# Performance work log

Measured on AMD Instinct MI355X. Metric: run time of the kernel, lower is better.

The kernel has to match this reference:

```python
import jax, jax.numpy as jnp
import numpy as np

RADIUS = 0.1
NSAMPLE = 32


def setup_inputs() -> dict:
    key = jax.random.key(0)
    k1, k2, k3, k4 = jax.random.split(key, 4)
    B, N, C = 8, 8192, 64
    C_in = 3 + C  # relative xyz concatenated with features
    H1, H2 = 64, 128
    xyz = jax.random.uniform(k1, (B, N, 3), dtype=jnp.float32)  # points in unit cube
    features = jax.random.normal(k2, (B, C, N), dtype=jnp.float32)
    W1 = jax.random.normal(k3, (H1, C_in), dtype=jnp.float32) / np.sqrt(C_in)
    b1 = jnp.zeros((H1,), dtype=jnp.float32)
    W2 = jax.random.normal(k4, (H2, H1), dtype=jnp.float32) / np.sqrt(H1)
    b2 = jnp.zeros((H2,), dtype=jnp.float32)
    return {"xyz": xyz, "features": features, "W1": W1, "b1": b1,
            "W2": W2, "b2": b2, "npoint": 2048}


def _ball_query(xyz, new_xyz, radius, nsample):
    # xyz: (B,N,3), new_xyz: (B,S,3) -> idx (B,S,nsample) int32
    N = xyz.shape[1]
    d2 = jnp.sum((new_xyz[:, :, None, :] - xyz[:, None, :, :]) ** 2, axis=-1)  # (B,S,N)
    mask = d2 < radius * radius
    # sort key: in-ball points keep their index (ascending order first),
    # out-of-ball points pushed behind by +N
    ar = jnp.arange(N, dtype=jnp.int32)
    key = jnp.where(mask, ar, ar + N)
    idx_sorted = jnp.argsort(key, axis=-1)[..., :nsample].astype(jnp.int32)  # (B,S,ns)
    count = jnp.sum(mask, axis=-1)  # (B,S)
    first = idx_sorted[..., :1]
    slot = jnp.arange(nsample)
    # CUDA ball_query pads missing slots with the first found index
    return jnp.where(slot[None, None, :] < count[..., None], idx_sorted, first)


def reference(xyz, features, W1, b1, W2, b2, npoint):
    # use_fps=False: sample_idxs = arange(npoint) -> new_xyz = first npoint points
    new_xyz = xyz[:, :npoint, :]  # (B,S,3)
    idx = _ball_query(xyz, new_xyz, RADIUS, NSAMPLE)  # (B,S,ns)

    # QueryAndGroup: gather xyz (centered) + features, concat on channel dim
    gx = jax.vmap(lambda p, i: p[i])(xyz, idx)  # (B,S,ns,3)
    rel = gx - new_xyz[:, :, None, :]  # (B,S,ns,3)
    gf = jax.vmap(lambda f, i: f[:, i])(features, idx)  # (B,C,S,ns)
    grouped = jnp.concatenate([jnp.transpose(rel, (0, 3, 1, 2)), gf], axis=1)  # (B,3+C,S,ns)

    # SharedMLP: 1x1 conv + ReLU stack
    h = jax.nn.relu(jnp.einsum('oc,bcsn->bosn', W1, grouped) + b1[None, :, None, None])
    h = jax.nn.relu(jnp.einsum('oc,bcsn->bosn', W2, h) + b2[None, :, None, None])

    # max_pool2d over nsample, squeeze
    new_features = jnp.max(h, axis=-1)  # (B,H2,S)
    return new_xyz, new_features
```

## Files before the change

### kernel.cpp

```cpp
#include <hip/hip_runtime.h>
#include <hip/hip_bf16.h>

#define B_      8
#define N_      8192
#define C_      64
#define H1_     64
#define H2_     128
#define NS      32
#define NPOINT  2048
#define NGROUP  (B_ * NPOINT)
#define NXYZ    (B_ * NPOINT * 3)
#define GD      10
#define NCP     1024

typedef short bf16x8 __attribute__((ext_vector_type(8)));
typedef short bf16x4 __attribute__((ext_vector_type(4)));
typedef float f32x4  __attribute__((ext_vector_type(4)));

#define MFMA32 __builtin_amdgcn_mfma_f32_16x16x32_bf16
#define MFMA16 __builtin_amdgcn_mfma_f32_16x16x16bf16_1k

__device__ inline unsigned short f2bf(float f) {
    unsigned u = __builtin_bit_cast(unsigned, f);
    return (unsigned short)((u + 0x7FFF + ((u >> 16) & 1)) >> 16);
}
__device__ inline float bf2f(unsigned short h) {
    unsigned u = ((unsigned)h) << 16;
    return __builtin_bit_cast(float, u);
}

__global__ __launch_bounds__(256) void copy_newxyz_kernel(
    const float* __restrict__ xyz, float* __restrict__ out)
{
    int i = blockIdx.x * 256 + threadIdx.x;
    if (i < NXYZ) {
        int b = i / (NPOINT * 3);
        int r = i - b * (NPOINT * 3);
        out[i] = xyz[(size_t)b * N_ * 3 + r];
    }
}

__global__ __launch_bounds__(256) void prep_kernel(
    const float* __restrict__ W1, const float* __restrict__ W2,
    unsigned short* __restrict__ W1x_hi, unsigned short* __restrict__ W1x_lo,
    unsigned short* __restrict__ W2x_hi, unsigned short* __restrict__ W2x_lo)
{
    int t = blockIdx.x * 256 + threadIdx.x;
    if (t < 6144) {
        int j = t & 7, cl = (t >> 3) & 15, kq = (t >> 7) & 3, t2 = t >> 9;
        int kt = t2 % 3, mt = t2 / 3;
        int row = mt * 16 + cl, k = kt * 32 + kq * 8 + j;
        float wv = 0.f;
        if (k < 64) wv = W1[row * 67 + 3 + k];
        else if (k < 67) wv = W1[row * 67 + (k - 64)];
        unsigned short h = f2bf(wv);
        W1x_hi[t] = h; W1x_lo[t] = f2bf(wv - bf2f(h));
    }
    if (t < 8192) {
        int i = t & 3, half = (t >> 2) & 1, cl = (t >> 3) & 15;
        int kq = (t >> 7) & 3, kt2p = (t >> 9) & 1, mt = t >> 10;
        int row = mt * 16 + cl, k = kt2p * 32 + half * 16 + kq * 4 + i;
        float wv = W2[row * 64 + k];
        unsigned short h = f2bf(wv);
        W2x_hi[t] = h; W2x_lo[t] = f2bf(wv - bf2f(h));
    }
}

__global__ __launch_bounds__(256) void ftrans_kernel(
    const float* __restrict__ f,
    unsigned short* __restrict__ hi, unsigned short* __restrict__ lo)
{
    __shared__ float tile[64][65];
    int bidx = blockIdx.x;
    int b = bidx >> 7, nt = bidx & 127;
    int n0 = nt * 64;
    int tx = threadIdx.x & 63, ty = threadIdx.x >> 6;
#pragma unroll
    for (int k = 0; k < 16; ++k) {
        int c = ty * 16 + k;
        tile[c][tx] = f[((size_t)b * C_ + c) * N_ + n0 + tx];
    }
    __syncthreads();
#pragma unroll
    for (int k = 0; k < 16; ++k) {
        int n = ty * 16 + k;
        float v = tile[tx][n];
        unsigned short h = f2bf(v);
        size_t dst = ((size_t)(b * N_ + n0 + n)) * C_ + tx;
        hi[dst] = h;
        lo[dst] = f2bf(v - bf2f(h));
    }
}

__global__ __launch_bounds__(256) void gridbuild_kernel(
    const float* __restrict__ xyz,
    int* __restrict__ cellStart,
    int* __restrict__ sortedId,
    float* __restrict__ sortedXyz)
{
    __shared__ int hist[NCP];
    __shared__ int wsum[4];
    int b = blockIdx.x, t = threadIdx.x;
    for (int i = t; i < NCP; i += 256) hist[i] = 0;
    __syncthreads();
    const float* base = xyz + (size_t)b * N_ * 3;
    for (int k = 0; k < N_ / 256; ++k) {
        int i = k * 256 + t;
        float x = base[i * 3], y = base[i * 3 + 1], z = base[i * 3 + 2];
        int c = (((int)(x * 9.999f)) * GD + (int)(y * 9.999f)) * GD + (int)(z * 9.999f);
        atomicAdd(&hist[c], 1);
    }
    __syncthreads();
    int h0 = hist[t * 4], h1 = hist[t * 4 + 1], h2 = hist[t * 4 + 2], h3 = hist[t * 4 + 3];
    int s = h0 + h1 + h2 + h3;
    int lane = t & 63, w = t >> 6;
    int v = s;
    for (int d = 1; d < 64; d <<= 1) {
        int o = __shfl_up(v, d);
        if (lane >= d) v += o;
    }
    if (lane == 63) wsum[w] = v;
    __syncthreads();
    int wofs = 0;
    for (int i = 0; i < 4; ++i) wofs += (i < w) ? wsum[i] : 0;
    int excl = wofs + v - s;
    int* cs = cellStart + b * (NCP + 1);
    cs[t * 4]     = excl;
    cs[t * 4 + 1] = excl + h0;
    cs[t * 4 + 2] = excl + h0 + h1;
    cs[t * 4 + 3] = excl + h0 + h1 + h2;
    if (t == 255) cs[NCP] = excl + s;
    __syncthreads();
    hist[t * 4] = excl; hist[t * 4 + 1] = excl + h0;
    hist[t * 4 + 2] = excl + h0 + h1; hist[t * 4 + 3] = excl + h0 + h1 + h2;
    __syncthreads();
    for (int k = 0; k < N_ / 256; ++k) {
        int i = k * 256 + t;
        float x = base[i * 3], y = base[i * 3 + 1], z = base[i * 3 + 2];
        int c = (((int)(x * 9.999f)) * GD + (int)(y * 9.999f)) * GD + (int)(z * 9.999f);
        int pos = atomicAdd(&hist[c], 1);
        sortedId[b * N_ + pos] = i;
        float* d = sortedXyz + ((size_t)(b * N_) + pos) * 3;
        d[0] = x; d[1] = y; d[2] = z;
    }
}

__global__ __launch_bounds__(256) void ballq_kernel(
    const float* __restrict__ xyz,
    const int* __restrict__ cellStart,
    const int* __restrict__ sortedId,
    const float* __restrict__ sortedXyz,
    int* __restrict__ idx)
{
    __shared__ int hitbuf[4][128];
    int t = threadIdx.x;
    int w = t >> 6, lane = t & 63;
    int g = blockIdx.x * 4 + w;
    int b = g >> 11, s = g & 2047;
    const float* qp = xyz + ((size_t)(b * N_) + s) * 3;
    float qx = qp[0], qy = qp[1], qz = qp[2];
    const float r2 = 0.01f;
    unsigned long long lmask = (1ull << lane) - 1ull;

    int cx = (int)(qx * 9.999f), cy = (int)(qy * 9.999f), cz = (int)(qz * 9.999f);
    int xlo = max(cx - 1, 0), xhi = min(cx + 1, GD - 1);
    int ylo = max(cy - 1, 0), yhi = min(cy + 1, GD - 1);
    int zlo = max(cz - 1, 0), zhi = min(cz + 1, GD - 1);
    int nx = xhi - xlo + 1, ny = yhi - ylo + 1;
    int nruns = nx * ny;

    const int* cs = cellStart + b * (NCP + 1);
    int start = 0, len = 0;
    if (lane < nruns) {
        int xi = xlo + lane / ny, yi = ylo + lane % ny;
        int cbase = (xi * GD + yi) * GD;
        start = cs[cbase + zlo];
        len = cs[cbase + zhi + 1] - start;
    }
    int v = len;
    for (int d = 1; d < 64; d <<= 1) {
        int o = __shfl_up(v, d);
        if (lane >= d) v += o;
    }
    int T = __shfl(v, 63);
    int excl = v - len;
    int ro[9], rs[9];
#pragma unroll
    for (int rr = 0; rr < 9; ++rr) {
        int oo = __shfl(excl, rr);
        int ss = __shfl(start, rr);
        bool live = rr < nruns;
        ro[rr] = live ? oo : 0x7fffffff;
        rs[rr] = live ? (ss - oo) : 0;
    }

    int cnt = 0;
    for (int k0 = 0; k0 < T; k0 += 64) {
        int pos = k0 + lane;
        bool valid = pos < T;
        int basev = rs[0];
#pragma unroll
        for (int rr = 1; rr < 9; ++rr)
            basev = (ro[rr] <= pos) ? rs[rr] : basev;
        float px = 1.e30f, py = 1.e30f, pz = 1.e30f;
        int pid = 0;
        if (valid) {
            int src = basev + pos;
            const float* pp = sortedXyz + ((size_t)(b * N_) + src) * 3;
            px = pp[0]; py = pp[1]; pz = pp[2];
            pid = sortedId[b * N_ + src];
        }
        float dx = __fsub_rn(px, qx);
        float dy = __fsub_rn(py, qy);
        float dz = __fsub_rn(pz, qz);
        float d2 = __fadd_rn(__fadd_rn(__fmul_rn(dx, dx), __fmul_rn(dy, dy)),
                             __fmul_rn(dz, dz));
        bool pred = valid && (d2 < r2);
        unsigned long long m = __ballot(pred);
        if (pred) {
            int p = cnt + __builtin_popcountll(m & lmask);
            if (p < 128) hitbuf[w][p] = pid;
        }
        cnt += __builtin_popcountll(m);
    }

    const int INF = 0x7fffffff;
    int v0 = (lane < cnt && lane < 128) ? hitbuf[w][lane] : INF;
    int v1 = (lane + 64 < cnt) ? hitbuf[w][lane + 64] : INF;
#pragma unroll
    for (int k = 2; k <= 128; k <<= 1) {
#pragma unroll
        for (int j = 64; j >= 1; j >>= 1) {
            if (j > (k >> 1)) continue;
            if (j == 64) {
                int lo = min(v0, v1), hi = max(v0, v1);
                v0 = lo; v1 = hi;
            } else {
                int p0 = __shfl_xor(v0, j), p1 = __shfl_xor(v1, j);
                bool lower = (lane & j) == 0;
                bool asc0 = (lane & k) == 0;
                bool asc1 = ((lane + 64) & k) == 0;
                v0 = (lower == asc0) ? min(v0, p0) : max(v0, p0);
                v1 = (lower == asc1) ? min(v1, p1) : max(v1, p1);
            }
        }
    }
    int first = __shfl(v0, 0);
    if (lane < NS) {
        int val = (lane < cnt) ? v0 : first;
        idx[(size_t)g * NS + lane] = val;
    }
}

__global__ __launch_bounds__(256) void mlp_mfma_kernel(
    const float* __restrict__ xyz,
    const unsigned short* __restrict__ fT_hi, const unsigned short* __restrict__ fT_lo,
    const unsigned short* __restrict__ W1x_hi, const unsigned short* __restrict__ W1x_lo,
    const float* __restrict__ b1,
    const unsigned short* __restrict__ W2x_hi, const unsigned short* __restrict__ W2x_lo,
    const float* __restrict__ b2,
    const int* __restrict__ idx,
    float* __restrict__ Ytmp)
{
    int t = threadIdx.x;
    int w = t >> 6, lane = t & 63;
    int g = blockIdx.x * 4 + w;
    int b = g >> 11, s = g & 2047;
    int cl = lane & 15, kq = lane >> 4;

    int i0 = idx[(size_t)g * NS + cl];
    int i1 = idx[(size_t)g * NS + 16 + cl];

    bf16x8 bh[2][2], bl[2][2];
#pragma unroll
    for (int nt = 0; nt < 2; ++nt) {
        int i = nt ? i1 : i0;
        size_t rowoff = ((size_t)(b * N_ + i)) * C_ + kq * 8;
#pragma unroll
        for (int kt = 0; kt < 2; ++kt) {
            bh[nt][kt] = *reinterpret_cast<const bf16x8*>(fT_hi + rowoff + kt * 32);
            bl[nt][kt] = *reinterpret_cast<const bf16x8*>(fT_lo + rowoff + kt * 32);
        }
    }
    const float* qp = xyz + ((size_t)(b * N_) + s) * 3;
    float qx = qp[0], qy = qp[1], qz = qp[2];
    bf16x8 brel[2];
#pragma unroll
    for (int nt = 0; nt < 2; ++nt) {
        int i = nt ? i1 : i0;
        bf16x8 vv = (bf16x8)(short)0;
        if (kq == 0) {
            const float* p = xyz + ((size_t)(b * N_) + i) * 3;
            vv[0] = (short)f2bf(__fsub_rn(p[0], qx));
            vv[1] = (short)f2bf(__fsub_rn(p[1], qy));
            vv[2] = (short)f2bf(__fsub_rn(p[2], qz));
        }
        brel[nt] = vv;
    }

    f32x4 acc[4][2];
#pragma unroll
    for (int mt = 0; mt < 4; ++mt) {
        f32x4 bias = *reinterpret_cast<const f32x4*>(b1 + mt * 16 + kq * 4);
        acc[mt][0] = bias;
        acc[mt][1] = bias;
    }
#pragma unroll
    for (int mt = 0; mt < 4; ++mt) {
        bf16x8 ah0 = *reinterpret_cast<const bf16x8*>(W1x_hi + (mt * 3 + 0) * 512 + lane * 8);
        bf16x8 ah1 = *reinterpret_cast<const bf16x8*>(W1x_hi + (mt * 3 + 1) * 512 + lane * 8);
        bf16x8 ah2 = *reinterpret_cast<const bf16x8*>(W1x_hi + (mt * 3 + 2) * 512 + lane * 8);
        bf16x8 al0 = *reinterpret_cast<const bf16x8*>(W1x_lo + (mt * 3 + 0) * 512 + lane * 8);
        bf16x8 al1 = *reinterpret_cast<const bf16x8*>(W1x_lo + (mt * 3 + 1) * 512 + lane * 8);
#pragma unroll
        for (int nt = 0; nt < 2; ++nt) {
            f32x4 a = acc[mt][nt];
            a = MFMA32(ah0, bh[nt][0], a, 0, 0, 0);
            a = MFMA32(ah0, bl[nt][0], a, 0, 0, 0);
            a = MFMA32(al0, bh[nt][0], a, 0, 0, 0);
            a = MFMA32(ah1, bh[nt][1], a, 0, 0, 0);
            a = MFMA32(ah1, bl[nt][1], a, 0, 0, 0);
            a = MFMA32(al1, bh[nt][1], a, 0, 0, 0);
            a = MFMA32(ah2, brel[nt], a, 0, 0, 0);
            acc[mt][nt] = a;
        }
    }

    bf16x4 p2h[4][2], p2l[4][2];
#pragma unroll
    for (int kt2 = 0; kt2 < 4; ++kt2)
#pragma unroll
        for (int nt = 0; nt < 2; ++nt) {
            f32x4 h = acc[kt2][nt];
            bf16x4 hh, hl;
#pragma unroll
            for (int i = 0; i < 4; ++i) {
                float hr = fmaxf(h[i], 0.f);
                unsigned short hb = f2bf(hr);
                hh[i] = (short)hb;
                hl[i] = (short)f2bf(hr - bf2f(hb));
            }
            p2h[kt2][nt] = hh;
            p2l[kt2][nt] = hl;
        }

#pragma unroll
    for (int hm = 0; hm < 2; ++hm) {
        f32x4 acc2[4][2];
#pragma unroll
        for (int mt4 = 0; mt4 < 4; ++mt4) {
            f32x4 bias = *reinterpret_cast<const f32x4*>(b2 + (hm * 4 + mt4) * 16 + kq * 4);
            acc2[mt4][0] = bias;
            acc2[mt4][1] = bias;
        }
#pragma unroll
        for (int mt4 = 0; mt4 < 4; ++mt4) {
            int mt = hm * 4 + mt4;
#pragma unroll
            for (int kt2p = 0; kt2p < 2; ++kt2p) {
                bf16x8 ah = *reinterpret_cast<const bf16x8*>(W2x_hi + (mt * 2 + kt2p) * 512 + lane * 8);
                bf16x8 al = *reinterpret_cast<const bf16x8*>(W2x_lo + (mt * 2 + kt2p) * 512 + lane * 8);
                bf16x4 ah_a = __builtin_shufflevector(ah, ah, 0, 1, 2, 3);
                bf16x4 ah_b = __builtin_shufflevector(ah, ah, 4, 5, 6, 7);
                bf16x4 al_a = __builtin_shufflevector(al, al, 0, 1, 2, 3);
                bf16x4 al_b = __builtin_shufflevector(al, al, 4, 5, 6, 7);
#pragma unroll
                for (int nt = 0; nt < 2; ++nt) {
                    f32x4 a = acc2[mt4][nt];
                    a = MFMA16(ah_a, p2h[kt2p * 2][nt], a, 0, 0, 0);
                    a = MFMA16(ah_a, p2l[kt2p * 2][nt], a, 0, 0, 0);
                    a = MFMA16(al_a, p2h[kt2p * 2][nt], a, 0, 0, 0);
                    a = MFMA16(ah_b, p2h[kt2p * 2 + 1][nt], a, 0, 0, 0);
                    a = MFMA16(ah_b, p2l[kt2p * 2 + 1][nt], a, 0, 0, 0);
                    a = MFMA16(al_b, p2h[kt2p * 2 + 1][nt], a, 0, 0, 0);
                    acc2[mt4][nt] = a;
                }
            }
        }
#pragma unroll
        for (int mt4 = 0; mt4 < 4; ++mt4) {
            f32x4 m;
#pragma unroll
            for (int r = 0; r < 4; ++r)
                m[r] = fmaxf(fmaxf(acc2[mt4][0][r], 0.f), fmaxf(acc2[mt4][1][r], 0.f));
#pragma unroll
            for (int mask = 1; mask <= 8; mask <<= 1)
#pragma unroll
                for (int r = 0; r < 4; ++r)
                    m[r] = fmaxf(m[r], __shfl_xor(m[r], mask));
            if (cl == 0)
                *reinterpret_cast<f32x4*>(Ytmp + (size_t)g * H2_ + (hm * 4 + mt4) * 16 + kq * 4) = m;
        }
    }
}

__global__ __launch_bounds__(256) void ytrans_kernel(
    const float* __restrict__ Y, float* __restrict__ out)
{
    __shared__ float tile[64][65];
    int blk = blockIdx.x;
    int b = blk >> 6, r = blk & 63;
    int st = r >> 1, ot = r & 1;
    int s0 = st * 64, o0 = ot * 64;
    int j = threadIdx.x & 63, i4 = threadIdx.x >> 6;
#pragma unroll
    for (int k = 0; k < 16; ++k) {
        int i = i4 * 16 + k;
        tile[i][j] = Y[((size_t)(b * NPOINT + s0 + i)) * H2_ + o0 + j];
    }
    __syncthreads();
#pragma unroll
    for (int k = 0; k < 16; ++k) {
        int i = i4 * 16 + k;
        out[NXYZ + ((size_t)(b * H2_ + o0 + i)) * NPOINT + s0 + j] = tile[j][i];
    }
}

extern "C" void kernel_launch(void* const* d_in, const int* in_sizes, int n_in,
                              void* d_out, int out_size, void* d_ws, size_t ws_size,
                              hipStream_t stream)
{
    const float* xyz  = (const float*)d_in[0];
    const float* feat = (const float*)d_in[1];
    const float* W1   = (const float*)d_in[2];
    const float* b1   = (const float*)d_in[3];
    const float* W2   = (const float*)d_in[4];
    const float* b2   = (const float*)d_in[5];
    float* out = (float*)d_out;

    char* ws = (char*)d_ws;
    size_t off = 0;
    int* idxbuf = (int*)(ws + off);                        off += (size_t)NGROUP * NS * 4;
    unsigned short* W1x_hi = (unsigned short*)(ws + off);  off += 6144 * 2;
    unsigned short* W1x_lo = (unsigned short*)(ws + off);  off += 6144 * 2;
    unsigned short* W2x_hi = (unsigned short*)(ws + off);  off += 8192 * 2;
    unsigned short* W2x_lo = (unsigned short*)(ws + off);  off += 8192 * 2;
    off = (off + 255) & ~(size_t)255;
    int* cellStart = (int*)(ws + off);                     off += (size_t)B_ * (NCP + 1) * 4;
    int* sortedId = (int*)(ws + off);                      off += (size_t)B_ * N_ * 4;
    float* sortedXyz = (float*)(ws + off);                 off += (size_t)B_ * N_ * 3 * 4;
    off = (off + 255) & ~(size_t)255;
    unsigned short* fT_hi = (unsigned short*)(ws + off);   off += (size_t)B_ * N_ * C_ * 2;
    unsigned short* fT_lo = (unsigned short*)(ws + off);   off += (size_t)B_ * N_ * C_ * 2;
    float* Ytmp = (float*)(ws + off);                      off += (size_t)NGROUP * H2_ * 4;

    copy_newxyz_kernel<<<(NXYZ + 255) / 256, 256, 0, stream>>>(xyz, out);
    prep_kernel<<<32, 256, 0, stream>>>(W1, W2, W1x_hi, W1x_lo, W2x_hi, W2x_lo);
    ftrans_kernel<<<B_ * (N_ / 64), 256, 0, stream>>>(feat, fT_hi, fT_lo);
    gridbuild_kernel<<<B_, 256, 0, stream>>>(xyz, cellStart, sortedId, sortedXyz);
    ballq_kernel<<<NGROUP / 4, 256, 0, stream>>>(xyz, cellStart, sortedId, sortedXyz, idxbuf);
    mlp_mfma_kernel<<<NGROUP / 4, 256, 0, stream>>>(
        xyz, fT_hi, fT_lo, W1x_hi, W1x_lo, b1, W2x_hi, W2x_lo, b2, idxbuf, Ytmp);
    ytrans_kernel<<<B_ * 64, 256, 0, stream>>>(Ytmp, out);
}
```

Before: 191.3 us.

## Fuse ball query, MLP and output transpose; merge prep kernels into one launch

```diff
diff --git a/kernel.cpp b/kernel.cpp
--- a/kernel.cpp
+++ b/kernel.cpp
@@ -29,134 +29,135 @@
     return __builtin_bit_cast(float, u);
 }
 
-__global__ __launch_bounds__(256) void copy_newxyz_kernel(
-    const float* __restrict__ xyz, float* __restrict__ out)
+__global__ __launch_bounds__(256) void prep_all_kernel(
+    const float* __restrict__ xyz, const float* __restrict__ feat,
+    const float* __restrict__ W1, const float* __restrict__ W2,
+    unsigned short* __restrict__ fT_hi, unsigned short* __restrict__ fT_lo,
+    int* __restrict__ cellStart, int* __restrict__ sortedId,
+    float* __restrict__ sortedXyz,
+    unsigned short* __restrict__ W1x_hi, unsigned short* __restrict__ W1x_lo,
+    unsigned short* __restrict__ W2x_hi, unsigned short* __restrict__ W2x_lo,
+    float* __restrict__ out)
 {
-    int i = blockIdx.x * 256 + threadIdx.x;
-    if (i < NXYZ) {
-        int b = i / (NPOINT * 3);
-        int r = i - b * (NPOINT * 3);
-        out[i] = xyz[(size_t)b * N_ * 3 + r];
+    __shared__ char smem[64 * 65 * 4];
+    int blk = blockIdx.x, t = threadIdx.x;
+
+    if (blk < 1024) {
+        float (*tile)[65] = reinterpret_cast<float(*)[65]>(smem);
+        int b = blk >> 7, nt = blk & 127;
+        int n0 = nt * 64;
+        int tx = t & 63, ty = t >> 6;
+#pragma unroll
+        for (int k = 0; k < 16; ++k) {
+            int c = ty * 16 + k;
+            tile[c][tx] = feat[((size_t)b * C_ + c) * N_ + n0 + tx];
+        }
+        __syncthreads();
+#pragma unroll
+        for (int k = 0; k < 16; ++k) {
+            int n = ty * 16 + k;
+            float v = tile[tx][n];
+            unsigned short h = f2bf(v);
+            size_t dst = ((size_t)(b * N_ + n0 + n)) * C_ + tx;
+            fT_hi[dst] = h;
+            fT_lo[dst] = f2bf(v - bf2f(h));
+        }
+    } else if (blk < 1032) {
+        int* hist = reinterpret_cast<int*>(smem);
+        int* wsum = hist + NCP;
+        int b = blk - 1024;
+        for (int i = t; i < NCP; i += 256) hist[i] = 0;
+        __syncthreads();
+        const float* base = xyz + (size_t)b * N_ * 3;
+        for (int k = 0; k < N_ / 256; ++k) {
+            int i = k * 256 + t;
+            float x = base[i * 3], y = base[i * 3 + 1], z = base[i * 3 + 2];
+            int c = (((int)(x * 9.999f)) * GD + (int)(y * 9.999f)) * GD + (int)(z * 9.999f);
+            atomicAdd(&hist[c], 1);
+        }
+        __syncthreads();
+        int h0 = hist[t * 4], h1 = hist[t * 4 + 1], h2 = hist[t * 4 + 2], h3 = hist[t * 4 + 3];
+        int s = h0 + h1 + h2 + h3;
+        int lane = t & 63, w = t >> 6;
+        int v = s;
+        for (int d = 1; d < 64; d <<= 1) {
+            int o = __shfl_up(v, d);
+            if (lane >= d) v += o;
+        }
+        if (lane == 63) wsum[w] = v;
+        __syncthreads();
+        int wofs = 0;
+        for (int i = 0; i < 4; ++i) wofs += (i < w) ? wsum[i] : 0;
+        int excl = wofs + v - s;
+        int* cs = cellStart + b * (NCP + 1);
+        cs[t * 4]     = excl;
+        cs[t * 4 + 1] = excl + h0;
+        cs[t * 4 + 2] = excl + h0 + h1;
+        cs[t * 4 + 3] = excl + h0 + h1 + h2;
+        if (t == 255) cs[NCP] = excl + s;
+        __syncthreads();
+        hist[t * 4] = excl; hist[t * 4 + 1] = excl + h0;
+        hist[t * 4 + 2] = excl + h0 + h1; hist[t * 4 + 3] = excl + h0 + h1 + h2;
+        __syncthreads();
+        for (int k = 0; k < N_ / 256; ++k) {
+            int i = k * 256 + t;
+            float x = base[i * 3], y = base[i * 3 + 1], z = base[i * 3 + 2];
+            int c = (((int)(x * 9.999f)) * GD + (int)(y * 9.999f)) * GD + (int)(z * 9.999f);
+            int pos = atomicAdd(&hist[c], 1);
+            sortedId[b * N_ + pos] = i;
+            float* d = sortedXyz + ((size_t)(b * N_) + pos) * 3;
+            d[0] = x; d[1] = y; d[2] = z;
+        }
+    } else if (blk < 1056) {
+        const float4* src = reinterpret_cast<const float4*>(xyz);
+        float4* dst = reinterpret_cast<float4*>(out);
+#pragma unroll
+        for (int k = 0; k < 2; ++k) {
+            int i4 = (blk - 1032) * 512 + k * 256 + t;
+            int b = i4 / 1536, r = i4 - b * 1536;
+            dst[i4] = src[b * 6144 + r];
+        }
+    } else {
+        int tg = (blk - 1056) * 256 + t;
+        if (tg < 6144) {
+            int j = tg & 7, cl = (tg >> 3) & 15, kq = (tg >> 7) & 3, t2 = tg >> 9;
+            int kt = t2 % 3, mt = t2 / 3;
+            int row = mt * 16 + cl, k = kt * 32 + kq * 8 + j;
+            float wv = 0.f;
+            if (k < 64) wv = W1[row * 67 + 3 + k];
+            else if (k < 67) wv = W1[row * 67 + (k - 64)];
+            unsigned short h = f2bf(wv);
+            W1x_hi[tg] = h; W1x_lo[tg] = f2bf(wv - bf2f(h));
+        }
+        if (tg < 8192) {
+            int i = tg & 3, half = (tg >> 2) & 1, cl = (tg >> 3) & 15;
+            int kq = (tg >> 7) & 3, kt2p = (tg >> 9) & 1, mt = tg >> 10;
+            int row = mt * 16 + cl, k = kt2p * 32 + half * 16 + kq * 4 + i;
+            float wv = W2[row * 64 + k];
+            unsigned short h = f2bf(wv);
+            W2x_hi[tg] = h; W2x_lo[tg] = f2bf(wv - bf2f(h));
+        }
     }
 }
 
-__global__ __launch_bounds__(256) void prep_kernel(
-    const float* __restrict__ W1, const float* __restrict__ W2,
-    unsigned short* __restrict__ W1x_hi, unsigned short* __restrict__ W1x_lo,
-    unsigned short* __restrict__ W2x_hi, unsigned short* __restrict__ W2x_lo)
-{
-    int t = blockIdx.x * 256 + threadIdx.x;
-    if (t < 6144) {
-        int j = t & 7, cl = (t >> 3) & 15, kq = (t >> 7) & 3, t2 = t >> 9;
-        int kt = t2 % 3, mt = t2 / 3;
-        int row = mt * 16 + cl, k = kt * 32 + kq * 8 + j;
-        float wv = 0.f;
-        if (k < 64) wv = W1[row * 67 + 3 + k];
-        else if (k < 67) wv = W1[row * 67 + (k - 64)];
-        unsigned short h = f2bf(wv);
-        W1x_hi[t] = h; W1x_lo[t] = f2bf(wv - bf2f(h));
-    }
-    if (t < 8192) {
-        int i = t & 3, half = (t >> 2) & 1, cl = (t >> 3) & 15;
-        int kq = (t >> 7) & 3, kt2p = (t >> 9) & 1, mt = t >> 10;
-        int row = mt * 16 + cl, k = kt2p * 32 + half * 16 + kq * 4 + i;
-        float wv = W2[row * 64 + k];
-        unsigned short h = f2bf(wv);
-        W2x_hi[t] = h; W2x_lo[t] = f2bf(wv - bf2f(h));
-    }
-}
-
-__global__ __launch_bounds__(256) void ftrans_kernel(
-    const float* __restrict__ f,
-    unsigned short* __restrict__ hi, unsigned short* __restrict__ lo)
-{
-    __shared__ float tile[64][65];
-    int bidx = blockIdx.x;
-    int b = bidx >> 7, nt = bidx & 127;
-    int n0 = nt * 64;
-    int tx = threadIdx.x & 63, ty = threadIdx.x >> 6;
-#pragma unroll
-    for (int k = 0; k < 16; ++k) {
-        int c = ty * 16 + k;
-        tile[c][tx] = f[((size_t)b * C_ + c) * N_ + n0 + tx];
-    }
-    __syncthreads();
-#pragma unroll
-    for (int k = 0; k < 16; ++k) {
-        int n = ty * 16 + k;
-        float v = tile[tx][n];
-        unsigned short h = f2bf(v);
-        size_t dst = ((size_t)(b * N_ + n0 + n)) * C_ + tx;
-        hi[dst] = h;
-        lo[dst] = f2bf(v - bf2f(h));
-    }
-}
-
-__global__ __launch_bounds__(256) void gridbuild_kernel(
-    const float* __restrict__ xyz,
-    int* __restrict__ cellStart,
-    int* __restrict__ sortedId,
-    float* __restrict__ sortedXyz)
-{
-    __shared__ int hist[NCP];
-    __shared__ int wsum[4];
-    int b = blockIdx.x, t = threadIdx.x;
-    for (int i = t; i < NCP; i += 256) hist[i] = 0;
-    __syncthreads();
-    const float* base = xyz + (size_t)b * N_ * 3;
-    for (int k = 0; k < N_ / 256; ++k) {
-        int i = k * 256 + t;
-        float x = base[i * 3], y = base[i * 3 + 1], z = base[i * 3 + 2];
-        int c = (((int)(x * 9.999f)) * GD + (int)(y * 9.999f)) * GD + (int)(z * 9.999f);
-        atomicAdd(&hist[c], 1);
-    }
-    __syncthreads();
-    int h0 = hist[t * 4], h1 = hist[t * 4 + 1], h2 = hist[t * 4 + 2], h3 = hist[t * 4 + 3];
-    int s = h0 + h1 + h2 + h3;
-    int lane = t & 63, w = t >> 6;
-    int v = s;
-    for (int d = 1; d < 64; d <<= 1) {
-        int o = __shfl_up(v, d);
-        if (lane >= d) v += o;
-    }
-    if (lane == 63) wsum[w] = v;
-    __syncthreads();
-    int wofs = 0;
-    for (int i = 0; i < 4; ++i) wofs += (i < w) ? wsum[i] : 0;
-    int excl = wofs + v - s;
-    int* cs = cellStart + b * (NCP + 1);
-    cs[t * 4]     = excl;
-    cs[t * 4 + 1] = excl + h0;
-    cs[t * 4 + 2] = excl + h0 + h1;
-    cs[t * 4 + 3] = excl + h0 + h1 + h2;
-    if (t == 255) cs[NCP] = excl + s;
-    __syncthreads();
-    hist[t * 4] = excl; hist[t * 4 + 1] = excl + h0;
-    hist[t * 4 + 2] = excl + h0 + h1; hist[t * 4 + 3] = excl + h0 + h1 + h2;
-    __syncthreads();
-    for (int k = 0; k < N_ / 256; ++k) {
-        int i = k * 256 + t;
-        float x = base[i * 3], y = base[i * 3 + 1], z = base[i * 3 + 2];
-        int c = (((int)(x * 9.999f)) * GD + (int)(y * 9.999f)) * GD + (int)(z * 9.999f);
-        int pos = atomicAdd(&hist[c], 1);
-        sortedId[b * N_ + pos] = i;
-        float* d = sortedXyz + ((size_t)(b * N_) + pos) * 3;
-        d[0] = x; d[1] = y; d[2] = z;
-    }
-}
-
-__global__ __launch_bounds__(256) void ballq_kernel(
+__global__ __launch_bounds__(256) void fused_kernel(
     const float* __restrict__ xyz,
     const int* __restrict__ cellStart,
     const int* __restrict__ sortedId,
     const float* __restrict__ sortedXyz,
-    int* __restrict__ idx)
+    const unsigned short* __restrict__ fT_hi, const unsigned short* __restrict__ fT_lo,
+    const unsigned short* __restrict__ W1x_hi, const unsigned short* __restrict__ W1x_lo,
+    const float* __restrict__ b1,
+    const unsigned short* __restrict__ W2x_hi, const unsigned short* __restrict__ W2x_lo,
+    const float* __restrict__ b2,
+    float* __restrict__ out)
 {
-    __shared__ int hitbuf[4][128];
+    __shared__ int shbuf[4][128];
     int t = threadIdx.x;
     int w = t >> 6, lane = t & 63;
     int g = blockIdx.x * 4 + w;
     int b = g >> 11, s = g & 2047;
+
     const float* qp = xyz + ((size_t)(b * N_) + s) * 3;
     float qx = qp[0], qy = qp[1], qz = qp[2];
     const float r2 = 0.01f;
@@ -219,14 +220,14 @@
         unsigned long long m = __ballot(pred);
         if (pred) {
             int p = cnt + __builtin_popcountll(m & lmask);
-            if (p < 128) hitbuf[w][p] = pid;
+            if (p < 128) shbuf[w][p] = pid;
         }
         cnt += __builtin_popcountll(m);
     }
 
     const int INF = 0x7fffffff;
-    int v0 = (lane < cnt && lane < 128) ? hitbuf[w][lane] : INF;
-    int v1 = (lane + 64 < cnt) ? hitbuf[w][lane + 64] : INF;
+    int v0 = (lane < cnt && lane < 128) ? shbuf[w][lane] : INF;
+    int v1 = (lane + 64 < cnt) ? shbuf[w][lane + 64] : INF;
 #pragma unroll
     for (int k = 2; k <= 128; k <<= 1) {
 #pragma unroll
@@ -246,30 +247,11 @@
         }
     }
     int first = __shfl(v0, 0);
-    if (lane < NS) {
-        int val = (lane < cnt) ? v0 : first;
-        idx[(size_t)g * NS + lane] = val;
-    }
-}
-
-__global__ __launch_bounds__(256) void mlp_mfma_kernel(
-    const float* __restrict__ xyz,
-    const unsigned short* __restrict__ fT_hi, const unsigned short* __restrict__ fT_lo,
-    const unsigned short* __restrict__ W1x_hi, const unsigned short* __restrict__ W1x_lo,
-    const float* __restrict__ b1,
-    const unsigned short* __restrict__ W2x_hi, const unsigned short* __restrict__ W2x_lo,
-    const float* __restrict__ b2,
-    const int* __restrict__ idx,
-    float* __restrict__ Ytmp)
-{
-    int t = threadIdx.x;
-    int w = t >> 6, lane = t & 63;
-    int g = blockIdx.x * 4 + w;
-    int b = g >> 11, s = g & 2047;
     int cl = lane & 15, kq = lane >> 4;
-
-    int i0 = idx[(size_t)g * NS + cl];
-    int i1 = idx[(size_t)g * NS + 16 + cl];
+    int sv0 = __shfl(v0, cl);
+    int sv1 = __shfl(v0, cl + 16);
+    int i0 = (cl < cnt) ? sv0 : first;
+    int i1 = (cl + 16 < cnt) ? sv1 : first;
 
     bf16x8 bh[2][2], bl[2][2];
 #pragma unroll
@@ -282,8 +264,6 @@
             bl[nt][kt] = *reinterpret_cast<const bf16x8*>(fT_lo + rowoff + kt * 32);
         }
     }
-    const float* qp = xyz + ((size_t)(b * N_) + s) * 3;
-    float qx = qp[0], qy = qp[1], qz = qp[2];
     bf16x8 brel[2];
 #pragma unroll
     for (int nt = 0; nt < 2; ++nt) {
@@ -344,6 +324,7 @@
             p2l[kt2][nt] = hl;
         }
 
+    float* ys = reinterpret_cast<float*>(&shbuf[0][0]);
 #pragma unroll
     for (int hm = 0; hm < 2; ++hm) {
         f32x4 acc2[4][2];
@@ -389,30 +370,17 @@
                 for (int r = 0; r < 4; ++r)
                     m[r] = fmaxf(m[r], __shfl_xor(m[r], mask));
             if (cl == 0)
-                *reinterpret_cast<f32x4*>(Ytmp + (size_t)g * H2_ + (hm * 4 + mt4) * 16 + kq * 4) = m;
-        }
-    }
-}
-
-__global__ __launch_bounds__(256) void ytrans_kernel(
-    const float* __restrict__ Y, float* __restrict__ out)
-{
-    __shared__ float tile[64][65];
-    int blk = blockIdx.x;
-    int b = blk >> 6, r = blk & 63;
-    int st = r >> 1, ot = r & 1;
-    int s0 = st * 64, o0 = ot * 64;
-    int j = threadIdx.x & 63, i4 = threadIdx.x >> 6;
-#pragma unroll
-    for (int k = 0; k < 16; ++k) {
-        int i = i4 * 16 + k;
-        tile[i][j] = Y[((size_t)(b * NPOINT + s0 + i)) * H2_ + o0 + j];
-    }
+                *reinterpret_cast<f32x4*>(ys + w * 128 + (hm * 4 + mt4) * 16 + kq * 4) = m;
+        }
+    }
+
     __syncthreads();
-#pragma unroll
-    for (int k = 0; k < 16; ++k) {
-        int i = i4 * 16 + k;
-        out[NXYZ + ((size_t)(b * H2_ + o0 + i)) * NPOINT + s0 + j] = tile[j][i];
+    if (t < 128) {
+        int o = t;
+        int bb = blockIdx.x >> 9;
+        int s0 = (blockIdx.x & 511) * 4;
+        float4 vv = { ys[0 * 128 + o], ys[1 * 128 + o], ys[2 * 128 + o], ys[3 * 128 + o] };
+        *reinterpret_cast<float4*>(out + NXYZ + ((size_t)(bb * H2_ + o)) * NPOINT + s0) = vv;
     }
 }
 
@@ -430,7 +398,6 @@
 
     char* ws = (char*)d_ws;
     size_t off = 0;
-    int* idxbuf = (int*)(ws + off);                        off += (size_t)NGROUP * NS * 4;
     unsigned short* W1x_hi = (unsigned short*)(ws + off);  off += 6144 * 2;
     unsigned short* W1x_lo = (unsigned short*)(ws + off);  off += 6144 * 2;
     unsigned short* W2x_hi = (unsigned short*)(ws + off);  off += 8192 * 2;
@@ -442,14 +409,11 @@
     off = (off + 255) & ~(size_t)255;
     unsigned short* fT_hi = (unsigned short*)(ws + off);   off += (size_t)B_ * N_ * C_ * 2;
     unsigned short* fT_lo = (unsigned short*)(ws + off);   off += (size_t)B_ * N_ * C_ * 2;
-    float* Ytmp = (float*)(ws + off);                      off += (size_t)NGROUP * H2_ * 4;
-
-    copy_newxyz_kernel<<<(NXYZ + 255) / 256, 256, 0, stream>>>(xyz, out);
-    prep_kernel<<<32, 256, 0, stream>>>(W1, W2, W1x_hi, W1x_lo, W2x_hi, W2x_lo);
-    ftrans_kernel<<<B_ * (N_ / 64), 256, 0, stream>>>(feat, fT_hi, fT_lo);
-    gridbuild_kernel<<<B_, 256, 0, stream>>>(xyz, cellStart, sortedId, sortedXyz);
-    ballq_kernel<<<NGROUP / 4, 256, 0, stream>>>(xyz, cellStart, sortedId, sortedXyz, idxbuf);
-    mlp_mfma_kernel<<<NGROUP / 4, 256, 0, stream>>>(
-        xyz, fT_hi, fT_lo, W1x_hi, W1x_lo, b1, W2x_hi, W2x_lo, b2, idxbuf, Ytmp);
-    ytrans_kernel<<<B_ * 64, 256, 0, stream>>>(Ytmp, out);
+
+    prep_all_kernel<<<1088, 256, 0, stream>>>(
+        xyz, feat, W1, W2, fT_hi, fT_lo, cellStart, sortedId, sortedXyz,
+        W1x_hi, W1x_lo, W2x_hi, W2x_lo, out);
+    fused_kernel<<<NGROUP / 4, 256, 0, stream>>>(
+        xyz, cellStart, sortedId, sortedXyz, fT_hi, fT_lo,
+        W1x_hi, W1x_lo, b1, W2x_hi, W2x_lo, b2, out);
 }
```

New measurement: 178.3 us. 6.8% less time.
